# Performance work log

Measured on AMD Instinct MI355X. Metric: run time of the kernel, lower is better.

The kernel has to match this reference:

```python
import jax, jax.numpy as jnp
import numpy as np

B, C, HW = 128, 3, 224
P = 16
D = 256
NH = 8
HD = D // NH
E = 4            # num_experts
K = 2            # top-k
FF = 4 * D
NC = 38
EPS = 1e-5


def _layernorm(x, g, b):
    mu = jnp.mean(x, axis=-1, keepdims=True)
    var = jnp.mean(jnp.square(x - mu), axis=-1, keepdims=True)
    return (x - mu) * jax.lax.rsqrt(var + EPS) * g + b


def setup_inputs() -> dict:
    key = jax.random.key(0)
    ks = jax.random.split(key, 16)
    s = 0.02
    return {
        "x": jax.random.normal(ks[0], (B, C, HW, HW), dtype=jnp.float32),
        "conv_w": jax.random.normal(ks[1], (D, C, P, P), dtype=jnp.float32) * s,
        "conv_b": jnp.zeros((D,), jnp.float32),
        "cls_token": jnp.zeros((1, 1, D), jnp.float32),
        "ln1_g": jnp.ones((D,), jnp.float32),
        "ln1_b": jnp.zeros((D,), jnp.float32),
        "qkv_w": jax.random.normal(ks[2], (3 * D, D), dtype=jnp.float32) * s,
        "qkv_b": jnp.zeros((3 * D,), jnp.float32),
        "out_w": jax.random.normal(ks[3], (D, D), dtype=jnp.float32) * s,
        "out_b": jnp.zeros((D,), jnp.float32),
        "ln2_g": jnp.ones((D,), jnp.float32),
        "ln2_b": jnp.zeros((D,), jnp.float32),
        "router_w": jax.random.normal(ks[4], (E, D), dtype=jnp.float32) * s,
        "router_b": jnp.zeros((E,), jnp.float32),
        "e_w1": jax.random.normal(ks[5], (E, D, FF), dtype=jnp.float32) * s,
        "e_b1": jnp.zeros((E, FF), jnp.float32),
        "e_w2": jax.random.normal(ks[6], (E, FF, D), dtype=jnp.float32) * s,
        "e_b2": jnp.zeros((E, D), jnp.float32),
        "head_w": jax.random.normal(ks[7], (NC, D), dtype=jnp.float32) * s,
        "head_b": jnp.zeros((NC,), jnp.float32),
    }


def reference(x, conv_w, conv_b, cls_token, ln1_g, ln1_b, qkv_w, qkv_b,
              out_w, out_b, ln2_g, ln2_b, router_w, router_b,
              e_w1, e_b1, e_w2, e_b2, head_w, head_b):
    # patch embed: Conv2d(3, D, 16, 16) -> [B, D, 14, 14] -> [B, 196, D]
    h = jax.lax.conv_general_dilated(
        x, conv_w, window_strides=(P, P), padding="VALID",
        dimension_numbers=("NCHW", "OIHW", "NCHW")) + conv_b[None, :, None, None]
    b = h.shape[0]
    tok = h.reshape(b, D, -1).transpose(0, 2, 1)            # [B, 196, D]
    tok = jnp.concatenate([jnp.broadcast_to(cls_token, (b, 1, D)), tok], axis=1)  # [B, 197, D]
    S = tok.shape[1]

    # Multi-head self-attention (pre-norm)
    x2 = _layernorm(tok, ln1_g, ln1_b)
    qkv = x2 @ qkv_w.T + qkv_b                              # [B, S, 3D]
    q, k, v = jnp.split(qkv, 3, axis=-1)
    q = q.reshape(b, S, NH, HD)
    k = k.reshape(b, S, NH, HD)
    v = v.reshape(b, S, NH, HD)
    scores = jnp.einsum("bqhd,bkhd->bhqk", q, k) / np.float32(np.sqrt(HD))
    attn = jax.nn.softmax(scores, axis=-1)
    ao = jnp.einsum("bhqk,bkhd->bqhd", attn, v).reshape(b, S, D)
    ao = ao @ out_w.T + out_b
    tok = tok + ao

    # MoE FFN (pre-norm). NOTE: original code computes top-k routing weights
    # but never multiplies outputs by them — outputs of selected experts are
    # simply summed. We reproduce that faithfully.
    x2 = _layernorm(tok, ln2_g, ln2_b)
    x_flat = x2.reshape(-1, D)                              # [T, D]
    logits = x_flat @ router_w.T + router_b                 # [T, E]
    probs = jax.nn.softmax(logits, axis=-1)
    _topw, topi = jax.lax.top_k(probs, K)                   # topw unused (as in source)
    mask = (topi[..., None] == jnp.arange(E)).any(axis=1)   # [T, E] bool
    out_flat = jnp.zeros_like(x_flat)
    for i in range(E):                                       # fixed small expert count
        hid = jax.nn.gelu(x_flat @ e_w1[i] + e_b1[i], approximate=False)
        out_flat = out_flat + mask[:, i:i + 1].astype(x_flat.dtype) * (hid @ e_w2[i] + e_b2[i])
    tok = tok + out_flat.reshape(b, S, D)

    return tok[:, 0] @ head_w.T + head_b                    # [B, NC]
```

## Files before the change

### kernel.cpp

```cpp
#include <hip/hip_runtime.h>
#include <hip/hip_bf16.h>
#include <math.h>

#define TTOK   25216
#define SEQL   197
#define NBATCH 128
#define DMODEL 256
#define NHEADS 8
#define FFD    1024
#define NEXP   4
#define NCLS   38
#define CONVK  768
#define NPATCH 196
#define CM     25088
#define KSPL   384

typedef unsigned short u16;
typedef unsigned int u32;
using s16x4 = __attribute__((ext_vector_type(4))) short;
using s16x8 = __attribute__((ext_vector_type(8))) short;
using f32x4 = __attribute__((ext_vector_type(4))) float;

__device__ __forceinline__ float b2f(u16 v) {
  union { unsigned u; float f; } x; x.u = (unsigned)v << 16; return x.f;
}
__device__ __forceinline__ u16 f2b(float f) {
  __hip_bfloat16 h = __float2bfloat16(f);
  return *reinterpret_cast<u16*>(&h);
}
__device__ __forceinline__ void gload16(const void* g, void* l) {
  __builtin_amdgcn_global_load_lds(
      (const __attribute__((address_space(1))) void*)g,
      (__attribute__((address_space(3))) void*)l, 16, 0, 0);
}
__device__ __forceinline__ float warp_sum(float v) {
  #pragma unroll
  for (int o = 32; o; o >>= 1) v += __shfl_xor(v, o);
  return v;
}
__device__ __forceinline__ float warp_max(float v) {
  #pragma unroll
  for (int o = 32; o; o >>= 1) v = fmaxf(v, __shfl_xor(v, o));
  return v;
}
__device__ __forceinline__ int fsw(int row) { return (row ^ (row >> 2)) & 3; }
__device__ __forceinline__ s16x8 ldA72(const u16* base, int rowa, int l4) {
  const char* p = (const char*)base + rowa * 72 + l4 * 16;
  s16x4 a = *(const s16x4*)p;
  s16x4 b = *(const s16x4*)(p + 8);
  return __builtin_shufflevector(a, b, 0, 1, 2, 3, 4, 5, 6, 7);
}

__global__ __launch_bounds__(256) void k_cast2b(const float* __restrict__ cw,
                                                u16* __restrict__ cwh,
                                                u16* __restrict__ cwl,
                                                const float* __restrict__ qw,
                                                u16* __restrict__ qwh,
                                                u16* __restrict__ qwl) {
  int bid = blockIdx.x;
  const float* in = cw; u16* hi = cwh; u16* lo = cwl;
  if (bid >= 192) { bid -= 192; in = qw; hi = qwh; lo = qwl; }
  int i = (bid * 256 + threadIdx.x) * 4;
  float4 v = *(const float4*)&in[i];
  float vv[4] = {v.x, v.y, v.z, v.w};
  u16 h[4], l[4];
  #pragma unroll
  for (int j = 0; j < 4; ++j) {
    h[j] = f2b(vv[j]);
    l[j] = f2b(vv[j] - b2f(h[j]));
  }
  *(uint2*)&hi[i] = *(const uint2*)h;
  *(uint2*)&lo[i] = *(const uint2*)l;
}

__global__ __launch_bounds__(256) void k_conv(const float* __restrict__ x,
                                              const u16* __restrict__ cwh,
                                              const u16* __restrict__ cwl,
                                              float* __restrict__ part) {
  const int n0 = blockIdx.x * 128;
  const int m0 = blockIdx.y * 128;
  const int kbase = blockIdx.z * KSPL;
  __shared__ __align__(16) u16 lds[25600];
  u16* Ah_s = lds;
  u16* Al_s = lds + 4608;
  u16* Wbuf = lds + 9216;
  const int tid = threadIdx.x;
  const int lane = tid & 63;
  const int wv = tid >> 6;
  const int wr = wv >> 1, wc = wv & 1;
  const int l15 = lane & 15, l4 = lane >> 4;
  f32x4 acc[4][4] = {};

  const int kpos = (tid & 7) * 4;
  long abase[4]; int aldso[4];
  #pragma unroll
  for (int it = 0; it < 4; ++it) {
    int row = it * 32 + (tid >> 3);
    int m = m0 + row;
    int b = m / NPATCH, p = m - b * NPATCH;
    int py = p / 14, px = p - py * 14;
    abase[it] = (long)(b * 3) * 50176 + (py * 16) * 224 + px * 16;
    aldso[it] = row * 72 + kpos * 2;
  }
  long woff[2]; int wofs[2];
  #pragma unroll
  for (int r = 0; r < 2; ++r) {
    int off = r * 4096 + tid * 16;
    int row = off >> 6;
    int c16 = (off >> 4) & 3;
    int kk = (c16 ^ fsw(row)) << 3;
    woff[r] = (long)(n0 + row) * CONVK + kbase + kk;
    wofs[r] = off;
  }
  #pragma unroll
  for (int r = 0; r < 2; ++r) {
    gload16(cwh + woff[r], (char*)Wbuf + wofs[r]);
    gload16(cwl + woff[r], (char*)Wbuf + 8192 + wofs[r]);
  }
  float4 xr[4];
  {
    int k = kbase + kpos;
    int c = k >> 8, r8 = k & 255;
    long soff = (long)c * 50176 + (r8 >> 4) * 224 + (r8 & 15);
    #pragma unroll
    for (int it = 0; it < 4; ++it) xr[it] = *(const float4*)&x[abase[it] + soff];
  }
  int cur = 0;
  for (int kc = 0; kc < KSPL; kc += 32) {
    #pragma unroll
    for (int it = 0; it < 4; ++it) {
      float vv[4] = {xr[it].x, xr[it].y, xr[it].z, xr[it].w};
      u16 h[4], l[4];
      #pragma unroll
      for (int j = 0; j < 4; ++j) {
        h[j] = f2b(vv[j]);
        l[j] = f2b(vv[j] - b2f(h[j]));
      }
      *(uint2*)((char*)Ah_s + aldso[it]) = *(const uint2*)h;
      *(uint2*)((char*)Al_s + aldso[it]) = *(const uint2*)l;
    }
    __syncthreads();
    if (kc + 32 < KSPL) {
      char* wdst = (char*)Wbuf + ((cur ^ 1) << 14);
      #pragma unroll
      for (int r = 0; r < 2; ++r) {
        gload16(cwh + woff[r] + kc + 32, wdst + wofs[r]);
        gload16(cwl + woff[r] + kc + 32, wdst + 8192 + wofs[r]);
      }
      int k = kbase + kc + 32 + kpos;
      int c = k >> 8, r8 = k & 255;
      long soff = (long)c * 50176 + (r8 >> 4) * 224 + (r8 & 15);
      #pragma unroll
      for (int it = 0; it < 4; ++it) xr[it] = *(const float4*)&x[abase[it] + soff];
    }
    const char* Wcur = (const char*)Wbuf + (cur << 14);
    s16x8 ah[4], al[4], bh[4], bl[4];
    #pragma unroll
    for (int i = 0; i < 4; ++i) {
      int rowa = wr * 64 + i * 16 + l15;
      ah[i] = ldA72(Ah_s, rowa, l4);
      al[i] = ldA72(Al_s, rowa, l4);
      int rowb = wc * 64 + i * 16 + l15;
      int kbb = (l4 ^ fsw(rowb)) << 4;
      bh[i] = *(const s16x8*)(Wcur + rowb * 64 + kbb);
      bl[i] = *(const s16x8*)(Wcur + 8192 + rowb * 64 + kbb);
    }
    #pragma unroll
    for (int i = 0; i < 4; ++i)
      #pragma unroll
      for (int j = 0; j < 4; ++j)
        acc[i][j] = __builtin_amdgcn_mfma_f32_16x16x32_bf16(ah[i], bh[j],
                                                            acc[i][j], 0, 0, 0);
    #pragma unroll
    for (int i = 0; i < 4; ++i)
      #pragma unroll
      for (int j = 0; j < 4; ++j)
        acc[i][j] = __builtin_amdgcn_mfma_f32_16x16x32_bf16(ah[i], bl[j],
                                                            acc[i][j], 0, 0, 0);
    #pragma unroll
    for (int i = 0; i < 4; ++i)
      #pragma unroll
      for (int j = 0; j < 4; ++j)
        acc[i][j] = __builtin_amdgcn_mfma_f32_16x16x32_bf16(al[i], bh[j],
                                                            acc[i][j], 0, 0, 0);
    __syncthreads();
    cur ^= 1;
  }
  float* pout = part + (size_t)blockIdx.z * CM * DMODEL;
  const int mb = m0 + wr * 64 + (l4 << 2);
  const int nb = n0 + wc * 64 + l15;
  #pragma unroll
  for (int i = 0; i < 4; ++i) {
    #pragma unroll
    for (int jf = 0; jf < 4; ++jf) {
      #pragma unroll
      for (int j = 0; j < 4; ++j) {
        int m = mb + i * 16 + j;
        int n = nb + jf * 16;
        pout[(long)m * DMODEL + n] = acc[i][jf][j];
      }
    }
  }
}

__global__ __launch_bounds__(256) void k_finish(const float* __restrict__ p0,
                                                const float* __restrict__ p1,
                                                const float* __restrict__ cb,
                                                const float* __restrict__ cls,
                                                float* __restrict__ tok,
                                                float2* __restrict__ st) {
  const int row = blockIdx.x * 4 + (threadIdx.x >> 6);
  const int lane = threadIdx.x & 63;
  const int b = row / SEQL, s = row - b * SEQL;
  float vv[4];
  if (s == 0) {
    *(float4*)vv = *(const float4*)&cls[lane * 4];
  } else {
    long m = (long)b * NPATCH + s - 1;
    float4 a = *(const float4*)&p0[m * DMODEL + lane * 4];
    float4 c = *(const float4*)&p1[m * DMODEL + lane * 4];
    float4 bi = *(const float4*)&cb[lane * 4];
    vv[0] = a.x + c.x + bi.x;
    vv[1] = a.y + c.y + bi.y;
    vv[2] = a.z + c.z + bi.z;
    vv[3] = a.w + c.w + bi.w;
  }
  *(float4*)&tok[(size_t)row * DMODEL + lane * 4] = *(const float4*)vv;
  float s1 = vv[0] + vv[1] + vv[2] + vv[3];
  float s2 = vv[0]*vv[0] + vv[1]*vv[1] + vv[2]*vv[2] + vv[3]*vv[3];
  s1 = warp_sum(s1);
  s2 = warp_sum(s2);
  if (lane == 0) {
    float mu = s1 * (1.f / DMODEL);
    float var = s2 * (1.f / DMODEL) - mu * mu;
    st[row] = make_float2(mu, rsqrtf(var + 1e-5f));
  }
}

__global__ __launch_bounds__(256) void k_qkv(const float* __restrict__ tok,
                                             const float2* __restrict__ stats,
                                             const float* __restrict__ g,
                                             const float* __restrict__ bb,
                                             const u16* __restrict__ Wh,
                                             const u16* __restrict__ Wl,
                                             const float* __restrict__ bias,
                                             float* __restrict__ Cf) {
  const int n0 = blockIdx.x * 128;
  const int m0 = blockIdx.y * 128;
  __shared__ __align__(16) u16 lds[25600];
  u16* Ah_s = lds;
  u16* Al_s = lds + 4608;
  u16* Wbuf = lds + 9216;
  const int tid = threadIdx.x;
  const int lane = tid & 63;
  const int wv = tid >> 6;
  const int wr = wv >> 1, wc = wv & 1;
  const int l15 = lane & 15, l4 = lane >> 4;
  f32x4 acc[4][4] = {};

  const int kpos = (tid & 7) * 4;
  long atok[4]; float2 st[4]; int aldso[4];
  #pragma unroll
  for (int it = 0; it < 4; ++it) {
    int row = it * 32 + (tid >> 3);
    int m = m0 + row;
    atok[it] = (long)m * DMODEL;
    st[it] = stats[m];
    aldso[it] = row * 72 + kpos * 2;
  }
  long woff[2]; int wofs[2];
  #pragma unroll
  for (int r = 0; r < 2; ++r) {
    int off = r * 4096 + tid * 16;
    int row = off >> 6;
    int c16 = (off >> 4) & 3;
    int kk = (c16 ^ fsw(row)) << 3;
    woff[r] = (long)(n0 + row) * DMODEL + kk;
    wofs[r] = off;
  }
  #pragma unroll
  for (int r = 0; r < 2; ++r) {
    gload16(Wh + woff[r], (char*)Wbuf + wofs[r]);
    gload16(Wl + woff[r], (char*)Wbuf + 8192 + wofs[r]);
  }
  float4 xr[4], gr, br;
  #pragma unroll
  for (int it = 0; it < 4; ++it) xr[it] = *(const float4*)&tok[atok[it] + kpos];
  gr = *(const float4*)&g[kpos];
  br = *(const float4*)&bb[kpos];
  int cur = 0;
  for (int kc = 0; kc < DMODEL; kc += 32) {
    float gg[4] = {gr.x, gr.y, gr.z, gr.w};
    float bbv[4] = {br.x, br.y, br.z, br.w};
    #pragma unroll
    for (int it = 0; it < 4; ++it) {
      float vv[4] = {xr[it].x, xr[it].y, xr[it].z, xr[it].w};
      u16 h[4], l[4];
      #pragma unroll
      for (int j = 0; j < 4; ++j) {
        float xd = (vv[j] - st[it].x) * st[it].y * gg[j] + bbv[j];
        h[j] = f2b(xd);
        l[j] = f2b(xd - b2f(h[j]));
      }
      *(uint2*)((char*)Ah_s + aldso[it]) = *(const uint2*)h;
      *(uint2*)((char*)Al_s + aldso[it]) = *(const uint2*)l;
    }
    __syncthreads();
    if (kc + 32 < DMODEL) {
      char* wdst = (char*)Wbuf + ((cur ^ 1) << 14);
      #pragma unroll
      for (int r = 0; r < 2; ++r) {
        gload16(Wh + woff[r] + kc + 32, wdst + wofs[r]);
        gload16(Wl + woff[r] + kc + 32, wdst + 8192 + wofs[r]);
      }
      #pragma unroll
      for (int it = 0; it < 4; ++it)
        xr[it] = *(const float4*)&tok[atok[it] + kc + 32 + kpos];
      gr = *(const float4*)&g[kc + 32 + kpos];
      br = *(const float4*)&bb[kc + 32 + kpos];
    }
    const char* Wcur = (const char*)Wbuf + (cur << 14);
    s16x8 ah[4], al[4], bh[4], bl[4];
    #pragma unroll
    for (int i = 0; i < 4; ++i) {
      int rowa = wr * 64 + i * 16 + l15;
      ah[i] = ldA72(Ah_s, rowa, l4);
      al[i] = ldA72(Al_s, rowa, l4);
      int rowb = wc * 64 + i * 16 + l15;
      int kbb = (l4 ^ fsw(rowb)) << 4;
      bh[i] = *(const s16x8*)(Wcur + rowb * 64 + kbb);
      bl[i] = *(const s16x8*)(Wcur + 8192 + rowb * 64 + kbb);
    }
    #pragma unroll
    for (int i = 0; i < 4; ++i)
      #pragma unroll
      for (int j = 0; j < 4; ++j)
        acc[i][j] = __builtin_amdgcn_mfma_f32_16x16x32_bf16(ah[i], bh[j],
                                                            acc[i][j], 0, 0, 0);
    #pragma unroll
    for (int i = 0; i < 4; ++i)
      #pragma unroll
      for (int j = 0; j < 4; ++j)
        acc[i][j] = __builtin_amdgcn_mfma_f32_16x16x32_bf16(ah[i], bl[j],
                                                            acc[i][j], 0, 0, 0);
    #pragma unroll
    for (int i = 0; i < 4; ++i)
      #pragma unroll
      for (int j = 0; j < 4; ++j)
        acc[i][j] = __builtin_amdgcn_mfma_f32_16x16x32_bf16(al[i], bh[j],
                                                            acc[i][j], 0, 0, 0);
    __syncthreads();
    cur ^= 1;
  }
  const int mb = m0 + wr * 64 + (l4 << 2);
  const int nb = n0 + wc * 64 + l15;
  #pragma unroll
  for (int i = 0; i < 4; ++i) {
    #pragma unroll
    for (int jf = 0; jf < 4; ++jf) {
      #pragma unroll
      for (int j = 0; j < 4; ++j) {
        int m = mb + i * 16 + j;
        int n = nb + jf * 16;
        Cf[(long)m * 512 + n] = acc[i][jf][j] + bias[n];
      }
    }
  }
}

__global__ __launch_bounds__(256) void k_qcls(const float* __restrict__ tok,
                                              const float2* __restrict__ stats,
                                              const float* __restrict__ g,
                                              const float* __restrict__ bb,
                                              const u16* __restrict__ qwh,
                                              const u16* __restrict__ qwl,
                                              const float* __restrict__ qb,
                                              u16* __restrict__ qch,
                                              u16* __restrict__ qcl) {
  const int b = blockIdx.x, n = threadIdx.x;
  __shared__ float xs[DMODEL];
  float2 st = stats[b * SEQL];
  float v = tok[(size_t)b * SEQL * DMODEL + n];
  xs[n] = (v - st.x) * st.y * g[n] + bb[n];
  __syncthreads();
  float val = qb[n];
  #pragma unroll 4
  for (int i = 0; i < 32; ++i) {
    s16x8 wh = *(const s16x8*)(qwh + (size_t)n * DMODEL + i * 8);
    s16x8 wl = *(const s16x8*)(qwl + (size_t)n * DMODEL + i * 8);
    #pragma unroll
    for (int j = 0; j < 8; ++j)
      val = fmaf(b2f((u16)wh[j]) + b2f((u16)wl[j]), xs[i * 8 + j], val);
  }
  u16 h = f2b(val);
  qch[b * DMODEL + n] = h;
  qcl[b * DMODEL + n] = f2b(val - b2f(h));
}

__global__ __launch_bounds__(256) void k_attn_cls(const u16* __restrict__ qch,
                                                  const u16* __restrict__ qcl,
                                                  const float* __restrict__ kvf,
                                                  float* __restrict__ ao) {
  const int w = threadIdx.x >> 6, lane = threadIdx.x & 63;
  const int unit = blockIdx.x * 4 + w;
  const int b = unit >> 3, h = unit & 7;
  __shared__ float Ss[4][200];
  float q[32];
  #pragma unroll
  for (int i = 0; i < 4; ++i) {
    s16x8 vh = *(const s16x8*)(qch + b * DMODEL + h * 32 + i * 8);
    s16x8 vl = *(const s16x8*)(qcl + b * DMODEL + h * 32 + i * 8);
    #pragma unroll
    for (int j = 0; j < 8; ++j) q[i * 8 + j] = b2f((u16)vh[j]) + b2f((u16)vl[j]);
  }
  float sc[4];
  float mx = -1e30f;
  #pragma unroll
  for (int r = 0; r < 4; ++r) {
    int k = lane + 64 * r;
    float s = -1e30f;
    if (k < SEQL) {
      const float* kr = kvf + ((size_t)(b * SEQL + k)) * 512 + h * 32;
      s = 0.f;
      #pragma unroll
      for (int i = 0; i < 8; ++i) {
        float4 kv4 = *(const float4*)(kr + i * 4);
        s = fmaf(kv4.x, q[i * 4 + 0], s);
        s = fmaf(kv4.y, q[i * 4 + 1], s);
        s = fmaf(kv4.z, q[i * 4 + 2], s);
        s = fmaf(kv4.w, q[i * 4 + 3], s);
      }
      s *= 0.17677669529663687f;
    }
    sc[r] = s;
    mx = fmaxf(mx, s);
  }
  mx = warp_max(mx);
  float sm = 0.f;
  #pragma unroll
  for (int r = 0; r < 4; ++r) {
    int k = lane + 64 * r;
    float e = (k < SEQL) ? __expf(sc[r] - mx) : 0.f;
    sc[r] = e;
    sm += e;
  }
  sm = warp_sum(sm);
  float inv = 1.f / sm;
  #pragma unroll
  for (int r = 0; r < 4; ++r) {
    int k = lane + 64 * r;
    if (k < SEQL) Ss[w][k] = sc[r] * inv;
  }
  int d = lane & 31, half = lane >> 5;
  float acc = 0.f;
  for (int i = 0; i < 99; ++i) {
    int k = half * 99 + i;
    if (k < SEQL)
      acc = fmaf(Ss[w][k], kvf[((size_t)(b * SEQL + k)) * 512 + 256 + h * 32 + d], acc);
  }
  acc += __shfl_xor(acc, 32);
  if (lane < 32) ao[(b * NHEADS + h) * 32 + d] = acc;
}

__global__ __launch_bounds__(256) void k_oproj_route(
    const float* __restrict__ ao, const float* __restrict__ ow,
    const float* __restrict__ ob, const float* __restrict__ tok,
    const float* __restrict__ g, const float* __restrict__ bb,
    const float* __restrict__ rw, const float* __restrict__ rb,
    float* __restrict__ tokc, float* __restrict__ x2cf,
    float* __restrict__ maskf) {
  const int b = blockIdx.x, n = threadIdx.x;
  const int w = n >> 6, lane = n & 63;
  __shared__ float xs[DMODEL];
  __shared__ float xd_s[DMODEL];
  __shared__ float red[8];
  __shared__ float lg[4];
  xs[n] = ao[b * DMODEL + n];
  __syncthreads();
  float val = ob[n];
  #pragma unroll 4
  for (int i = 0; i < 64; ++i) {
    float4 wv = *(const float4*)(ow + (size_t)n * DMODEL + i * 4);
    val = fmaf(wv.x, xs[i * 4 + 0], val);
    val = fmaf(wv.y, xs[i * 4 + 1], val);
    val = fmaf(wv.z, xs[i * 4 + 2], val);
    val = fmaf(wv.w, xs[i * 4 + 3], val);
  }
  float t = tok[(size_t)b * SEQL * DMODEL + n] + val;
  tokc[b * DMODEL + n] = t;
  float s1 = warp_sum(t), s2 = warp_sum(t * t);
  if (lane == 0) { red[w] = s1; red[4 + w] = s2; }
  __syncthreads();
  s1 = red[0] + red[1] + red[2] + red[3];
  s2 = red[4] + red[5] + red[6] + red[7];
  float mu = s1 * (1.f / DMODEL);
  float var = s2 * (1.f / DMODEL) - mu * mu;
  float rs = rsqrtf(var + 1e-5f);
  float xd = (t - mu) * rs * g[n] + bb[n];
  x2cf[b * DMODEL + n] = xd;
  xd_s[n] = xd;
  __syncthreads();
  float s = 0.f;
  #pragma unroll
  for (int i = 0; i < 4; ++i) s = fmaf(xd_s[lane + i * 64], rw[w * DMODEL + lane + i * 64], s);
  s = warp_sum(s) + rb[w];
  if (lane == 0) lg[w] = s;
  __syncthreads();
  if (n < NEXP) {
    int e = n;
    int rank = 0;
    #pragma unroll
    for (int j = 0; j < NEXP; ++j)
      if (j != e && (lg[j] > lg[e] || (lg[j] == lg[e] && j < e))) ++rank;
    maskf[b * NEXP + e] = (rank < 2) ? 1.f : 0.f;
  }
}

__global__ __launch_bounds__(256) void k_moe1(const float* __restrict__ x2cf,
                                              const float* __restrict__ w1,
                                              const float* __restrict__ b1,
                                              const float* __restrict__ maskf,
                                              float* __restrict__ hid) {
  const int e = blockIdx.x, t = blockIdx.y;
  if (maskf[t * NEXP + e] == 0.f) return;
  __shared__ float xs[DMODEL];
  const int tid = threadIdx.x;
  xs[tid] = x2cf[t * DMODEL + tid];
  __syncthreads();
  const float* w1e = w1 + (size_t)e * DMODEL * FFD + tid;
  float a0 = 0.f, a1 = 0.f, a2 = 0.f, a3 = 0.f;
  #pragma unroll 4
  for (int k = 0; k < DMODEL; ++k) {
    float xv = xs[k];
    const float* wr_ = w1e + (size_t)k * FFD;
    a0 = fmaf(xv, wr_[0], a0);
    a1 = fmaf(xv, wr_[256], a1);
    a2 = fmaf(xv, wr_[512], a2);
    a3 = fmaf(xv, wr_[768], a3);
  }
  float accs[4] = {a0, a1, a2, a3};
  float* hrow = hid + ((size_t)e * NBATCH + t) * FFD;
  #pragma unroll
  for (int j = 0; j < 4; ++j) {
    float v = accs[j] + b1[e * FFD + tid + j * 256];
    hrow[tid + j * 256] = 0.5f * v * (1.0f + erff(v * 0.70710678118654752f));
  }
}

__global__ __launch_bounds__(256) void k_moe2(const float* __restrict__ hid,
                                              const float* __restrict__ w2,
                                              const float* __restrict__ b2,
                                              const float* __restrict__ maskf,
                                              float* __restrict__ tokc) {
  const int t = blockIdx.x, dc = blockIdx.y;
  const int tid = threadIdx.x;
  const int dl = tid & 127, kh = tid >> 7;
  const int dout = dc * 128 + dl;
  int e0 = 0;
  while (e0 < 3 && maskf[t * NEXP + e0] == 0.f) ++e0;
  int e1 = e0 + 1;
  while (e1 < 3 && maskf[t * NEXP + e1] == 0.f) ++e1;
  __shared__ float hs0[FFD], hs1[FFD];
  const float* h0 = hid + ((size_t)e0 * NBATCH + t) * FFD;
  const float* h1 = hid + ((size_t)e1 * NBATCH + t) * FFD;
  for (int i = tid * 4; i < FFD; i += 1024) {
    *(float4*)&hs0[i] = *(const float4*)&h0[i];
    *(float4*)&hs1[i] = *(const float4*)&h1[i];
  }
  __syncthreads();
  const float* w20 = w2 + (size_t)e0 * FFD * DMODEL + dout;
  const float* w21 = w2 + (size_t)e1 * FFD * DMODEL + dout;
  float a0 = 0.f, a1 = 0.f;
  const int k0 = kh * 512;
  #pragma unroll 8
  for (int k = k0; k < k0 + 512; ++k) {
    a0 = fmaf(hs0[k], w20[(size_t)k * DMODEL], a0);
    a1 = fmaf(hs1[k], w21[(size_t)k * DMODEL], a1);
  }
  __shared__ float red[256];
  red[tid] = a0 + a1;
  __syncthreads();
  if (kh == 0) {
    float full = red[dl] + red[128 + dl] +
                 b2[e0 * DMODEL + dout] + b2[e1 * DMODEL + dout];
    tokc[t * DMODEL + dout] += full;
  }
}

__global__ __launch_bounds__(256) void k_head(const float* __restrict__ tokc,
                                              const float* __restrict__ hw,
                                              const float* __restrict__ hb,
                                              float* __restrict__ out) {
  int b = blockIdx.x;
  int w = threadIdx.x >> 6, lane = threadIdx.x & 63;
  const float* row = tokc + (size_t)b * DMODEL;
  for (int c = w; c < NCLS; c += 4) {
    float s = 0.f;
    for (int d = lane; d < DMODEL; d += 64) s = fmaf(row[d], hw[c * DMODEL + d], s);
    s = warp_sum(s);
    if (lane == 0) out[b * NCLS + c] = s + hb[c];
  }
}

extern "C" void kernel_launch(void* const* d_in, const int* in_sizes, int n_in,
                              void* d_out, int out_size, void* d_ws, size_t ws_size,
                              hipStream_t stream) {
  const float* x      = (const float*)d_in[0];
  const float* conv_w = (const float*)d_in[1];
  const float* conv_b = (const float*)d_in[2];
  const float* cls    = (const float*)d_in[3];
  const float* ln1g   = (const float*)d_in[4];
  const float* ln1b   = (const float*)d_in[5];
  const float* qkv_w  = (const float*)d_in[6];
  const float* qkv_b  = (const float*)d_in[7];
  const float* out_w  = (const float*)d_in[8];
  const float* out_b  = (const float*)d_in[9];
  const float* ln2g   = (const float*)d_in[10];
  const float* ln2b   = (const float*)d_in[11];
  const float* rw     = (const float*)d_in[12];
  const float* rb     = (const float*)d_in[13];
  const float* e_w1   = (const float*)d_in[14];
  const float* e_b1   = (const float*)d_in[15];
  const float* e_w2   = (const float*)d_in[16];
  const float* e_b2   = (const float*)d_in[17];
  const float* head_w = (const float*)d_in[18];
  const float* head_b = (const float*)d_in[19];
  float* out = (float*)d_out;

  char* ws = (char*)d_ws;
  size_t off = 0;
  auto alloc = [&](size_t bytes) {
    void* p = ws + off;
    off += (bytes + 255) & ~(size_t)255;
    return p;
  };
  float*  tok   = (float*)alloc((size_t)TTOK * DMODEL * 4);
  float*  qkvf  = (float*)alloc((size_t)TTOK * 512 * 4);
  float2* stats = (float2*)alloc((size_t)TTOK * 8);
  u16*    cwh   = (u16*)alloc((size_t)DMODEL * CONVK * 2);
  u16*    cwl   = (u16*)alloc((size_t)DMODEL * CONVK * 2);
  u16*    qwh   = (u16*)alloc((size_t)768 * DMODEL * 2);
  u16*    qwl   = (u16*)alloc((size_t)768 * DMODEL * 2);
  u16*    qch   = (u16*)alloc((size_t)NBATCH * DMODEL * 2);
  u16*    qcl   = (u16*)alloc((size_t)NBATCH * DMODEL * 2);
  float*  aocf  = (float*)alloc((size_t)NBATCH * DMODEL * 4);
  float*  tokc  = (float*)alloc((size_t)NBATCH * DMODEL * 4);
  float*  x2cf  = (float*)alloc((size_t)NBATCH * DMODEL * 4);
  float*  maskf = (float*)alloc((size_t)NBATCH * NEXP * 4);
  float*  hid   = (float*)alloc((size_t)NEXP * NBATCH * FFD * 4);
  float* part = qkvf;

  k_cast2b<<<384, 256, 0, stream>>>(conv_w, cwh, cwl, qkv_w, qwh, qwl);

  k_conv<<<dim3(2, CM / 128, 2), 256, 0, stream>>>(x, cwh, cwl, part);

  k_finish<<<TTOK / 4, 256, 0, stream>>>(part, part + (size_t)CM * DMODEL,
                                         conv_b, cls, tok, stats);

  k_qkv<<<dim3(4, TTOK / 128), 256, 0, stream>>>(
      tok, stats, ln1g, ln1b, qwh + 256 * DMODEL, qwl + 256 * DMODEL,
      qkv_b + 256, qkvf);

  k_qcls<<<NBATCH, 256, 0, stream>>>(tok, stats, ln1g, ln1b, qwh, qwl, qkv_b,
                                     qch, qcl);

  k_attn_cls<<<NBATCH * NHEADS / 4, 256, 0, stream>>>(qch, qcl, qkvf, aocf);

  k_oproj_route<<<NBATCH, 256, 0, stream>>>(aocf, out_w, out_b, tok,
                                            ln2g, ln2b, rw, rb,
                                            tokc, x2cf, maskf);

  k_moe1<<<dim3(NEXP, NBATCH), 256, 0, stream>>>(x2cf, e_w1, e_b1, maskf, hid);
  k_moe2<<<dim3(NBATCH, 2), 256, 0, stream>>>(hid, e_w2, e_b2, maskf, tokc);

  k_head<<<NBATCH, 256, 0, stream>>>(tokc, head_w, head_b, out);
}
```

Baseline: 214.7 us.

## Fuse conv bias into conv GEMM, load A fragments from registers, share CLS query

The conv GEMM drops its split-K partial buffers and writes biased tokens straight into the token tensor, so the finish pass only copies the CLS token and computes LayerNorm stats. Both GEMMs now build bf16 hi/lo A fragments directly in registers from global loads instead of staging them through LDS, and use 64-row tiles. Because the CLS token is the same for every batch, the CLS query is computed once by a single block and shared, and the o-proj reads cls directly. This removes a partial-buffer round trip and the A-tile LDS traffic, at the cost of uncoalesced per-lane global loads for A and smaller tiles that reuse the weights less.

```diff
diff --git a/kernel.cpp b/kernel.cpp
--- a/kernel.cpp
+++ b/kernel.cpp
@@ -13,11 +13,9 @@
 #define CONVK  768
 #define NPATCH 196
 #define CM     25088
-#define KSPL   384
 
 typedef unsigned short u16;
 typedef unsigned int u32;
-using s16x4 = __attribute__((ext_vector_type(4))) short;
 using s16x8 = __attribute__((ext_vector_type(8))) short;
 using f32x4 = __attribute__((ext_vector_type(4))) float;
 
@@ -44,11 +42,15 @@
   return v;
 }
 __device__ __forceinline__ int fsw(int row) { return (row ^ (row >> 2)) & 3; }
-__device__ __forceinline__ s16x8 ldA72(const u16* base, int rowa, int l4) {
-  const char* p = (const char*)base + rowa * 72 + l4 * 16;
-  s16x4 a = *(const s16x4*)p;
-  s16x4 b = *(const s16x4*)(p + 8);
-  return __builtin_shufflevector(a, b, 0, 1, 2, 3, 4, 5, 6, 7);
+__device__ __forceinline__ void split8(const float* vv, s16x8* hi, s16x8* lo) {
+  u16 h[8], l[8];
+  #pragma unroll
+  for (int j = 0; j < 8; ++j) {
+    h[j] = f2b(vv[j]);
+    l[j] = f2b(vv[j] - b2f(h[j]));
+  }
+  *hi = *(const s16x8*)h;
+  *lo = *(const s16x8*)l;
 }
 
 __global__ __launch_bounds__(256) void k_cast2b(const float* __restrict__ cw,
@@ -76,31 +78,25 @@
 __global__ __launch_bounds__(256) void k_conv(const float* __restrict__ x,
                                               const u16* __restrict__ cwh,
                                               const u16* __restrict__ cwl,
-                                              float* __restrict__ part) {
+                                              const float* __restrict__ cb,
+                                              float* __restrict__ tok) {
   const int n0 = blockIdx.x * 128;
-  const int m0 = blockIdx.y * 128;
-  const int kbase = blockIdx.z * KSPL;
-  __shared__ __align__(16) u16 lds[25600];
-  u16* Ah_s = lds;
-  u16* Al_s = lds + 4608;
-  u16* Wbuf = lds + 9216;
+  const int m0 = blockIdx.y * 64;
+  __shared__ __align__(16) u16 Wbuf[2 * 8192];
   const int tid = threadIdx.x;
   const int lane = tid & 63;
   const int wv = tid >> 6;
   const int wr = wv >> 1, wc = wv & 1;
   const int l15 = lane & 15, l4 = lane >> 4;
-  f32x4 acc[4][4] = {};
-
-  const int kpos = (tid & 7) * 4;
-  long abase[4]; int aldso[4];
-  #pragma unroll
-  for (int it = 0; it < 4; ++it) {
-    int row = it * 32 + (tid >> 3);
-    int m = m0 + row;
+  f32x4 acc[2][4] = {};
+
+  long mb8[2];
+  #pragma unroll
+  for (int i = 0; i < 2; ++i) {
+    int m = m0 + wr * 32 + i * 16 + l15;
     int b = m / NPATCH, p = m - b * NPATCH;
     int py = p / 14, px = p - py * 14;
-    abase[it] = (long)(b * 3) * 50176 + (py * 16) * 224 + px * 16;
-    aldso[it] = row * 72 + kpos * 2;
+    mb8[i] = (long)(b * 3) * 50176 + (py * 16) * 224 + px * 16;
   }
   long woff[2]; int wofs[2];
   #pragma unroll
@@ -109,7 +105,7 @@
     int row = off >> 6;
     int c16 = (off >> 4) & 3;
     int kk = (c16 ^ fsw(row)) << 3;
-    woff[r] = (long)(n0 + row) * CONVK + kbase + kk;
+    woff[r] = (long)(n0 + row) * CONVK + kk;
     wofs[r] = off;
   }
   #pragma unroll
@@ -117,96 +113,98 @@
     gload16(cwh + woff[r], (char*)Wbuf + wofs[r]);
     gload16(cwl + woff[r], (char*)Wbuf + 8192 + wofs[r]);
   }
-  float4 xr[4];
+  float4 xa[2][2];
   {
-    int k = kbase + kpos;
+    int k = l4 * 8;
     int c = k >> 8, r8 = k & 255;
-    long soff = (long)c * 50176 + (r8 >> 4) * 224 + (r8 & 15);
-    #pragma unroll
-    for (int it = 0; it < 4; ++it) xr[it] = *(const float4*)&x[abase[it] + soff];
-  }
+    long soff = (long)c * 50176 + ((r8 >> 4) * 224) + (r8 & 15);
+    #pragma unroll
+    for (int i = 0; i < 2; ++i) {
+      xa[i][0] = *(const float4*)&x[mb8[i] + soff];
+      xa[i][1] = *(const float4*)&x[mb8[i] + soff + 4];
+    }
+  }
+  __syncthreads();
   int cur = 0;
-  for (int kc = 0; kc < KSPL; kc += 32) {
-    #pragma unroll
-    for (int it = 0; it < 4; ++it) {
-      float vv[4] = {xr[it].x, xr[it].y, xr[it].z, xr[it].w};
-      u16 h[4], l[4];
-      #pragma unroll
-      for (int j = 0; j < 4; ++j) {
-        h[j] = f2b(vv[j]);
-        l[j] = f2b(vv[j] - b2f(h[j]));
-      }
-      *(uint2*)((char*)Ah_s + aldso[it]) = *(const uint2*)h;
-      *(uint2*)((char*)Al_s + aldso[it]) = *(const uint2*)l;
-    }
-    __syncthreads();
-    if (kc + 32 < KSPL) {
-      char* wdst = (char*)Wbuf + ((cur ^ 1) << 14);
+  for (int kc = 0; kc < CONVK; kc += 32) {
+    float4 xb[2][2];
+    if (kc + 32 < CONVK) {
+      char* wdst = (char*)Wbuf + ((cur ^ 1) * 16384);
       #pragma unroll
       for (int r = 0; r < 2; ++r) {
         gload16(cwh + woff[r] + kc + 32, wdst + wofs[r]);
         gload16(cwl + woff[r] + kc + 32, wdst + 8192 + wofs[r]);
       }
-      int k = kbase + kc + 32 + kpos;
+      int k = kc + 32 + l4 * 8;
       int c = k >> 8, r8 = k & 255;
-      long soff = (long)c * 50176 + (r8 >> 4) * 224 + (r8 & 15);
-      #pragma unroll
-      for (int it = 0; it < 4; ++it) xr[it] = *(const float4*)&x[abase[it] + soff];
-    }
-    const char* Wcur = (const char*)Wbuf + (cur << 14);
-    s16x8 ah[4], al[4], bh[4], bl[4];
-    #pragma unroll
-    for (int i = 0; i < 4; ++i) {
-      int rowa = wr * 64 + i * 16 + l15;
-      ah[i] = ldA72(Ah_s, rowa, l4);
-      al[i] = ldA72(Al_s, rowa, l4);
-      int rowb = wc * 64 + i * 16 + l15;
+      long soff = (long)c * 50176 + ((r8 >> 4) * 224) + (r8 & 15);
+      #pragma unroll
+      for (int i = 0; i < 2; ++i) {
+        xb[i][0] = *(const float4*)&x[mb8[i] + soff];
+        xb[i][1] = *(const float4*)&x[mb8[i] + soff + 4];
+      }
+    }
+    s16x8 ah[2], al[2];
+    #pragma unroll
+    for (int i = 0; i < 2; ++i) {
+      float vv[8] = {xa[i][0].x, xa[i][0].y, xa[i][0].z, xa[i][0].w,
+                     xa[i][1].x, xa[i][1].y, xa[i][1].z, xa[i][1].w};
+      split8(vv, &ah[i], &al[i]);
+    }
+    const char* Wcur = (const char*)Wbuf + cur * 16384;
+    s16x8 bh[4], bl[4];
+    #pragma unroll
+    for (int j = 0; j < 4; ++j) {
+      int rowb = wc * 64 + j * 16 + l15;
       int kbb = (l4 ^ fsw(rowb)) << 4;
-      bh[i] = *(const s16x8*)(Wcur + rowb * 64 + kbb);
-      bl[i] = *(const s16x8*)(Wcur + 8192 + rowb * 64 + kbb);
-    }
-    #pragma unroll
-    for (int i = 0; i < 4; ++i)
+      bh[j] = *(const s16x8*)(Wcur + rowb * 64 + kbb);
+      bl[j] = *(const s16x8*)(Wcur + 8192 + rowb * 64 + kbb);
+    }
+    #pragma unroll
+    for (int i = 0; i < 2; ++i)
       #pragma unroll
       for (int j = 0; j < 4; ++j)
         acc[i][j] = __builtin_amdgcn_mfma_f32_16x16x32_bf16(ah[i], bh[j],
                                                             acc[i][j], 0, 0, 0);
     #pragma unroll
-    for (int i = 0; i < 4; ++i)
+    for (int i = 0; i < 2; ++i)
       #pragma unroll
       for (int j = 0; j < 4; ++j)
         acc[i][j] = __builtin_amdgcn_mfma_f32_16x16x32_bf16(ah[i], bl[j],
                                                             acc[i][j], 0, 0, 0);
     #pragma unroll
-    for (int i = 0; i < 4; ++i)
+    for (int i = 0; i < 2; ++i)
       #pragma unroll
       for (int j = 0; j < 4; ++j)
         acc[i][j] = __builtin_amdgcn_mfma_f32_16x16x32_bf16(al[i], bh[j],
                                                             acc[i][j], 0, 0, 0);
     __syncthreads();
     cur ^= 1;
-  }
-  float* pout = part + (size_t)blockIdx.z * CM * DMODEL;
-  const int mb = m0 + wr * 64 + (l4 << 2);
+    #pragma unroll
+    for (int i = 0; i < 2; ++i) {
+      xa[i][0] = xb[i][0];
+      xa[i][1] = xb[i][1];
+    }
+  }
+  const int mb = m0 + wr * 32 + (l4 << 2);
   const int nb = n0 + wc * 64 + l15;
   #pragma unroll
-  for (int i = 0; i < 4; ++i) {
+  for (int i = 0; i < 2; ++i) {
     #pragma unroll
     for (int jf = 0; jf < 4; ++jf) {
       #pragma unroll
       for (int j = 0; j < 4; ++j) {
         int m = mb + i * 16 + j;
         int n = nb + jf * 16;
-        pout[(long)m * DMODEL + n] = acc[i][jf][j];
+        int bq = m / NPATCH;
+        long cr = (long)bq * SEQL + (m - bq * NPATCH) + 1;
+        tok[cr * DMODEL + n] = acc[i][jf][j] + cb[n];
       }
     }
   }
 }
 
-__global__ __launch_bounds__(256) void k_finish(const float* __restrict__ p0,
-                                                const float* __restrict__ p1,
-                                                const float* __restrict__ cb,
-                                                const float* __restrict__ cls,
+__global__ __launch_bounds__(256) void k_lnstat(const float* __restrict__ cls,
                                                 float* __restrict__ tok,
                                                 float2* __restrict__ st) {
   const int row = blockIdx.x * 4 + (threadIdx.x >> 6);
@@ -215,17 +213,10 @@
   float vv[4];
   if (s == 0) {
     *(float4*)vv = *(const float4*)&cls[lane * 4];
+    *(float4*)&tok[(size_t)row * DMODEL + lane * 4] = *(const float4*)vv;
   } else {
-    long m = (long)b * NPATCH + s - 1;
-    float4 a = *(const float4*)&p0[m * DMODEL + lane * 4];
-    float4 c = *(const float4*)&p1[m * DMODEL + lane * 4];
-    float4 bi = *(const float4*)&cb[lane * 4];
-    vv[0] = a.x + c.x + bi.x;
-    vv[1] = a.y + c.y + bi.y;
-    vv[2] = a.z + c.z + bi.z;
-    vv[3] = a.w + c.w + bi.w;
-  }
-  *(float4*)&tok[(size_t)row * DMODEL + lane * 4] = *(const float4*)vv;
+    *(float4*)vv = *(const float4*)&tok[(size_t)row * DMODEL + lane * 4];
+  }
   float s1 = vv[0] + vv[1] + vv[2] + vv[3];
   float s2 = vv[0]*vv[0] + vv[1]*vv[1] + vv[2]*vv[2] + vv[3]*vv[3];
   s1 = warp_sum(s1);
@@ -246,27 +237,21 @@
                                              const float* __restrict__ bias,
                                              float* __restrict__ Cf) {
   const int n0 = blockIdx.x * 128;
-  const int m0 = blockIdx.y * 128;
-  __shared__ __align__(16) u16 lds[25600];
-  u16* Ah_s = lds;
-  u16* Al_s = lds + 4608;
-  u16* Wbuf = lds + 9216;
+  const int m0 = blockIdx.y * 64;
+  __shared__ __align__(16) u16 Wbuf[2 * 8192];
   const int tid = threadIdx.x;
   const int lane = tid & 63;
   const int wv = tid >> 6;
   const int wr = wv >> 1, wc = wv & 1;
   const int l15 = lane & 15, l4 = lane >> 4;
-  f32x4 acc[4][4] = {};
-
-  const int kpos = (tid & 7) * 4;
-  long atok[4]; float2 st[4]; int aldso[4];
-  #pragma unroll
-  for (int it = 0; it < 4; ++it) {
-    int row = it * 32 + (tid >> 3);
-    int m = m0 + row;
-    atok[it] = (long)m * DMODEL;
-    st[it] = stats[m];
-    aldso[it] = row * 72 + kpos * 2;
+  f32x4 acc[2][4] = {};
+
+  long atok[2]; float2 st[2];
+  #pragma unroll
+  for (int i = 0; i < 2; ++i) {
+    int m = m0 + wr * 32 + i * 16 + l15;
+    atok[i] = (long)m * DMODEL;
+    st[i] = stats[m];
   }
   long woff[2]; int wofs[2];
   #pragma unroll
@@ -283,79 +268,93 @@
     gload16(Wh + woff[r], (char*)Wbuf + wofs[r]);
     gload16(Wl + woff[r], (char*)Wbuf + 8192 + wofs[r]);
   }
-  float4 xr[4], gr, br;
-  #pragma unroll
-  for (int it = 0; it < 4; ++it) xr[it] = *(const float4*)&tok[atok[it] + kpos];
-  gr = *(const float4*)&g[kpos];
-  br = *(const float4*)&bb[kpos];
+  float4 xa[2][2], ga[2], ba[2];
+  {
+    int k = l4 * 8;
+    #pragma unroll
+    for (int i = 0; i < 2; ++i) {
+      xa[i][0] = *(const float4*)&tok[atok[i] + k];
+      xa[i][1] = *(const float4*)&tok[atok[i] + k + 4];
+    }
+    ga[0] = *(const float4*)&g[k];  ga[1] = *(const float4*)&g[k + 4];
+    ba[0] = *(const float4*)&bb[k]; ba[1] = *(const float4*)&bb[k + 4];
+  }
+  __syncthreads();
   int cur = 0;
   for (int kc = 0; kc < DMODEL; kc += 32) {
-    float gg[4] = {gr.x, gr.y, gr.z, gr.w};
-    float bbv[4] = {br.x, br.y, br.z, br.w};
-    #pragma unroll
-    for (int it = 0; it < 4; ++it) {
-      float vv[4] = {xr[it].x, xr[it].y, xr[it].z, xr[it].w};
-      u16 h[4], l[4];
-      #pragma unroll
-      for (int j = 0; j < 4; ++j) {
-        float xd = (vv[j] - st[it].x) * st[it].y * gg[j] + bbv[j];
-        h[j] = f2b(xd);
-        l[j] = f2b(xd - b2f(h[j]));
-      }
-      *(uint2*)((char*)Ah_s + aldso[it]) = *(const uint2*)h;
-      *(uint2*)((char*)Al_s + aldso[it]) = *(const uint2*)l;
-    }
-    __syncthreads();
+    float4 xb[2][2], gb[2], bbv[2];
     if (kc + 32 < DMODEL) {
-      char* wdst = (char*)Wbuf + ((cur ^ 1) << 14);
+      char* wdst = (char*)Wbuf + ((cur ^ 1) * 16384);
       #pragma unroll
       for (int r = 0; r < 2; ++r) {
         gload16(Wh + woff[r] + kc + 32, wdst + wofs[r]);
         gload16(Wl + woff[r] + kc + 32, wdst + 8192 + wofs[r]);
       }
-      #pragma unroll
-      for (int it = 0; it < 4; ++it)
-        xr[it] = *(const float4*)&tok[atok[it] + kc + 32 + kpos];
-      gr = *(const float4*)&g[kc + 32 + kpos];
-      br = *(const float4*)&bb[kc + 32 + kpos];
-    }
-    const char* Wcur = (const char*)Wbuf + (cur << 14);
-    s16x8 ah[4], al[4], bh[4], bl[4];
-    #pragma unroll
-    for (int i = 0; i < 4; ++i) {
-      int rowa = wr * 64 + i * 16 + l15;
-      ah[i] = ldA72(Ah_s, rowa, l4);
-      al[i] = ldA72(Al_s, rowa, l4);
-      int rowb = wc * 64 + i * 16 + l15;
+      int k = kc + 32 + l4 * 8;
+      #pragma unroll
+      for (int i = 0; i < 2; ++i) {
+        xb[i][0] = *(const float4*)&tok[atok[i] + k];
+        xb[i][1] = *(const float4*)&tok[atok[i] + k + 4];
+      }
+      gb[0] = *(const float4*)&g[k];  gb[1] = *(const float4*)&g[k + 4];
+      bbv[0] = *(const float4*)&bb[k]; bbv[1] = *(const float4*)&bb[k + 4];
+    }
+    s16x8 ah[2], al[2];
+    float gg[8] = {ga[0].x, ga[0].y, ga[0].z, ga[0].w,
+                   ga[1].x, ga[1].y, ga[1].z, ga[1].w};
+    float bv[8] = {ba[0].x, ba[0].y, ba[0].z, ba[0].w,
+                   ba[1].x, ba[1].y, ba[1].z, ba[1].w};
+    #pragma unroll
+    for (int i = 0; i < 2; ++i) {
+      float raw[8] = {xa[i][0].x, xa[i][0].y, xa[i][0].z, xa[i][0].w,
+                      xa[i][1].x, xa[i][1].y, xa[i][1].z, xa[i][1].w};
+      float vv[8];
+      #pragma unroll
+      for (int j = 0; j < 8; ++j)
+        vv[j] = (raw[j] - st[i].x) * st[i].y * gg[j] + bv[j];
+      split8(vv, &ah[i], &al[i]);
+    }
+    const char* Wcur = (const char*)Wbuf + cur * 16384;
+    s16x8 bh[4], bl[4];
+    #pragma unroll
+    for (int j = 0; j < 4; ++j) {
+      int rowb = wc * 64 + j * 16 + l15;
       int kbb = (l4 ^ fsw(rowb)) << 4;
-      bh[i] = *(const s16x8*)(Wcur + rowb * 64 + kbb);
-      bl[i] = *(const s16x8*)(Wcur + 8192 + rowb * 64 + kbb);
-    }
-    #pragma unroll
-    for (int i = 0; i < 4; ++i)
+      bh[j] = *(const s16x8*)(Wcur + rowb * 64 + kbb);
+      bl[j] = *(const s16x8*)(Wcur + 8192 + rowb * 64 + kbb);
+    }
+    #pragma unroll
+    for (int i = 0; i < 2; ++i)
       #pragma unroll
       for (int j = 0; j < 4; ++j)
         acc[i][j] = __builtin_amdgcn_mfma_f32_16x16x32_bf16(ah[i], bh[j],
                                                             acc[i][j], 0, 0, 0);
     #pragma unroll
-    for (int i = 0; i < 4; ++i)
+    for (int i = 0; i < 2; ++i)
       #pragma unroll
       for (int j = 0; j < 4; ++j)
         acc[i][j] = __builtin_amdgcn_mfma_f32_16x16x32_bf16(ah[i], bl[j],
                                                             acc[i][j], 0, 0, 0);
     #pragma unroll
-    for (int i = 0; i < 4; ++i)
+    for (int i = 0; i < 2; ++i)
       #pragma unroll
       for (int j = 0; j < 4; ++j)
         acc[i][j] = __builtin_amdgcn_mfma_f32_16x16x32_bf16(al[i], bh[j],
                                                             acc[i][j], 0, 0, 0);
     __syncthreads();
     cur ^= 1;
-  }
-  const int mb = m0 + wr * 64 + (l4 << 2);
+    #pragma unroll
+    for (int i = 0; i < 2; ++i) {
+      xa[i][0] = xb[i][0];
+      xa[i][1] = xb[i][1];
+    }
+    ga[0] = gb[0]; ga[1] = gb[1];
+    ba[0] = bbv[0]; ba[1] = bbv[1];
+  }
+  const int mb = m0 + wr * 32 + (l4 << 2);
   const int nb = n0 + wc * 64 + l15;
   #pragma unroll
-  for (int i = 0; i < 4; ++i) {
+  for (int i = 0; i < 2; ++i) {
     #pragma unroll
     for (int jf = 0; jf < 4; ++jf) {
       #pragma unroll
@@ -368,20 +367,26 @@
   }
 }
 
-__global__ __launch_bounds__(256) void k_qcls(const float* __restrict__ tok,
-                                              const float2* __restrict__ stats,
-                                              const float* __restrict__ g,
-                                              const float* __restrict__ bb,
-                                              const u16* __restrict__ qwh,
-                                              const u16* __restrict__ qwl,
-                                              const float* __restrict__ qb,
-                                              u16* __restrict__ qch,
-                                              u16* __restrict__ qcl) {
-  const int b = blockIdx.x, n = threadIdx.x;
+__global__ __launch_bounds__(256) void k_qcls1(const float* __restrict__ cls,
+                                               const float* __restrict__ g,
+                                               const float* __restrict__ bb,
+                                               const u16* __restrict__ qwh,
+                                               const u16* __restrict__ qwl,
+                                               const float* __restrict__ qb,
+                                               float* __restrict__ qf) {
+  const int n = threadIdx.x, w = n >> 6, lane = n & 63;
   __shared__ float xs[DMODEL];
-  float2 st = stats[b * SEQL];
-  float v = tok[(size_t)b * SEQL * DMODEL + n];
-  xs[n] = (v - st.x) * st.y * g[n] + bb[n];
+  __shared__ float red[8];
+  float v = cls[n];
+  float s1 = warp_sum(v), s2 = warp_sum(v * v);
+  if (lane == 0) { red[w] = s1; red[4 + w] = s2; }
+  __syncthreads();
+  s1 = red[0] + red[1] + red[2] + red[3];
+  s2 = red[4] + red[5] + red[6] + red[7];
+  float mu = s1 * (1.f / DMODEL);
+  float var = s2 * (1.f / DMODEL) - mu * mu;
+  float rs = rsqrtf(var + 1e-5f);
+  xs[n] = (v - mu) * rs * g[n] + bb[n];
   __syncthreads();
   float val = qb[n];
   #pragma unroll 4
@@ -392,13 +397,10 @@
     for (int j = 0; j < 8; ++j)
       val = fmaf(b2f((u16)wh[j]) + b2f((u16)wl[j]), xs[i * 8 + j], val);
   }
-  u16 h = f2b(val);
-  qch[b * DMODEL + n] = h;
-  qcl[b * DMODEL + n] = f2b(val - b2f(h));
-}
-
-__global__ __launch_bounds__(256) void k_attn_cls(const u16* __restrict__ qch,
-                                                  const u16* __restrict__ qcl,
+  qf[n] = val;
+}
+
+__global__ __launch_bounds__(256) void k_attn_cls(const float* __restrict__ qf,
                                                   const float* __restrict__ kvf,
                                                   float* __restrict__ ao) {
   const int w = threadIdx.x >> 6, lane = threadIdx.x & 63;
@@ -407,11 +409,10 @@
   __shared__ float Ss[4][200];
   float q[32];
   #pragma unroll
-  for (int i = 0; i < 4; ++i) {
-    s16x8 vh = *(const s16x8*)(qch + b * DMODEL + h * 32 + i * 8);
-    s16x8 vl = *(const s16x8*)(qcl + b * DMODEL + h * 32 + i * 8);
-    #pragma unroll
-    for (int j = 0; j < 8; ++j) q[i * 8 + j] = b2f((u16)vh[j]) + b2f((u16)vl[j]);
+  for (int i = 0; i < 8; ++i) {
+    float4 q4 = *(const float4*)(qf + h * 32 + i * 4);
+    q[i * 4 + 0] = q4.x; q[i * 4 + 1] = q4.y;
+    q[i * 4 + 2] = q4.z; q[i * 4 + 3] = q4.w;
   }
   float sc[4];
   float mx = -1e30f;
@@ -464,7 +465,7 @@
 
 __global__ __launch_bounds__(256) void k_oproj_route(
     const float* __restrict__ ao, const float* __restrict__ ow,
-    const float* __restrict__ ob, const float* __restrict__ tok,
+    const float* __restrict__ ob, const float* __restrict__ cls,
     const float* __restrict__ g, const float* __restrict__ bb,
     const float* __restrict__ rw, const float* __restrict__ rb,
     float* __restrict__ tokc, float* __restrict__ x2cf,
@@ -486,7 +487,7 @@
     val = fmaf(wv.z, xs[i * 4 + 2], val);
     val = fmaf(wv.w, xs[i * 4 + 3], val);
   }
-  float t = tok[(size_t)b * SEQL * DMODEL + n] + val;
+  float t = cls[n] + val;
   tokc[b * DMODEL + n] = t;
   float s1 = warp_sum(t), s2 = warp_sum(t * t);
   if (lane == 0) { red[w] = s1; red[4 + w] = s2; }
@@ -641,32 +642,28 @@
   u16*    cwl   = (u16*)alloc((size_t)DMODEL * CONVK * 2);
   u16*    qwh   = (u16*)alloc((size_t)768 * DMODEL * 2);
   u16*    qwl   = (u16*)alloc((size_t)768 * DMODEL * 2);
-  u16*    qch   = (u16*)alloc((size_t)NBATCH * DMODEL * 2);
-  u16*    qcl   = (u16*)alloc((size_t)NBATCH * DMODEL * 2);
+  float*  qf    = (float*)alloc((size_t)DMODEL * 4);
   float*  aocf  = (float*)alloc((size_t)NBATCH * DMODEL * 4);
   float*  tokc  = (float*)alloc((size_t)NBATCH * DMODEL * 4);
   float*  x2cf  = (float*)alloc((size_t)NBATCH * DMODEL * 4);
   float*  maskf = (float*)alloc((size_t)NBATCH * NEXP * 4);
   float*  hid   = (float*)alloc((size_t)NEXP * NBATCH * FFD * 4);
-  float* part = qkvf;
 
   k_cast2b<<<384, 256, 0, stream>>>(conv_w, cwh, cwl, qkv_w, qwh, qwl);
 
-  k_conv<<<dim3(2, CM / 128, 2), 256, 0, stream>>>(x, cwh, cwl, part);
-
-  k_finish<<<TTOK / 4, 256, 0, stream>>>(part, part + (size_t)CM * DMODEL,
-                                         conv_b, cls, tok, stats);
-
-  k_qkv<<<dim3(4, TTOK / 128), 256, 0, stream>>>(
+  k_conv<<<dim3(2, CM / 64), 256, 0, stream>>>(x, cwh, cwl, conv_b, tok);
+
+  k_lnstat<<<TTOK / 4, 256, 0, stream>>>(cls, tok, stats);
+
+  k_qkv<<<dim3(4, TTOK / 64), 256, 0, stream>>>(
       tok, stats, ln1g, ln1b, qwh + 256 * DMODEL, qwl + 256 * DMODEL,
       qkv_b + 256, qkvf);
 
-  k_qcls<<<NBATCH, 256, 0, stream>>>(tok, stats, ln1g, ln1b, qwh, qwl, qkv_b,
-                                     qch, qcl);
-
-  k_attn_cls<<<NBATCH * NHEADS / 4, 256, 0, stream>>>(qch, qcl, qkvf, aocf);
-
-  k_oproj_route<<<NBATCH, 256, 0, stream>>>(aocf, out_w, out_b, tok,
+  k_qcls1<<<1, 256, 0, stream>>>(cls, ln1g, ln1b, qwh, qwl, qkv_b, qf);
+
+  k_attn_cls<<<NBATCH * NHEADS / 4, 256, 0, stream>>>(qf, qkvf, aocf);
+
+  k_oproj_route<<<NBATCH, 256, 0, stream>>>(aocf, out_w, out_b, cls,
                                             ln2g, ln2b, rw, rb,
                                             tokc, x2cf, maskf);
 
```

New measurement: 239.8 us. 11.7% more time.
